# Optimization experiments

Hardware: AMD Instinct MI355X
Metric: run time of the kernel (lower is better)

The kernel has to match this reference:

```python
import jax, jax.numpy as jnp
import numpy as np

B, D = 8192, 256
NUM_CLASSES = 128
CHUNK = 256          # matches module chunk_size; B % CHUNK == 0
TEMP = 0.07
EPS_NORM = 1e-12


def setup_inputs() -> dict:
    key = jax.random.key(0)
    k1, k2 = jax.random.split(key)
    features = jax.random.normal(k1, (B, D), dtype=jnp.float32)
    labels = jax.random.randint(k2, (B,), 0, NUM_CLASSES, dtype=jnp.int64)
    return {"features": features, "labels": labels}


def reference(features, labels):
    n = features.shape[0]
    temperature = max(TEMP, 1e-4)

    # F.normalize(dim=1): x / max(||x||, eps)
    norm = jnp.maximum(jnp.linalg.norm(features, axis=1, keepdims=True), EPS_NORM)
    f = features / norm
    # clamp is a no-op after normalization but kept for faithfulness
    f = jnp.clip(f, -1000.0, 1000.0)

    # [B, B] similarity; the torch loop computes exactly these rows chunk by chunk
    sim = jnp.matmul(f, f.T) / temperature

    # self-mask: each row i masks column i (diagonal of its chunk's square block)
    self_mask = ~jnp.eye(n, dtype=bool)

    # positive mask: same label, excluding self
    pos = (labels[:, None] == labels[None, :]) & self_mask
    # per-chunk fallback: if a 256-row chunk has no positives at all, use self_mask
    pos_c = pos.reshape(n // CHUNK, CHUNK, n)
    has_pos = pos_c.any(axis=(1, 2), keepdims=True)
    pos = jnp.where(has_pos, pos_c, self_mask.reshape(n // CHUNK, CHUNK, n)).reshape(n, n)

    # max-subtract BEFORE self-masking (faithful: includes self-sim = 1/temp)
    sim_max = jnp.max(sim, axis=1, keepdims=True)
    logits = jnp.clip(sim - jax.lax.stop_gradient(sim_max), -1000.0, 1000.0)

    exp_sim = jnp.maximum(jnp.exp(logits), 1e-8) * self_mask
    log_sum_exp = jnp.log(jnp.sum(exp_sim, axis=1, keepdims=True) + 1e-8)
    log_prob = jnp.maximum(logits - log_sum_exp, -1000.0)

    pos_pairs = jnp.sum(pos, axis=1)                      # [B] int
    row_loss = -jnp.sum(pos * log_prob, axis=1)           # [B]
    valid = pos_pairs > 0
    row_loss = jnp.where(valid, row_loss / jnp.maximum(pos_pairs, 1).astype(row_loss.dtype), 0.0)

    total_loss = jnp.sum(row_loss)
    total_pairs = jnp.sum(valid).astype(jnp.float32)
    mean_loss = total_loss / (total_pairs + 1e-8)
    loss = mean_loss  # reduction == 'mean'
    return loss, total_pairs, mean_loss
```

## Files before the change

kernel.cpp:

```cpp
#include <hip/hip_runtime.h>
#include <hip/hip_bf16.h>

#define NB 8192
#define DD 256
#define INV_T (1.0f/0.07f)
#define LOG2E 1.4426950408889634f
#define K1    (INV_T*LOG2E)
#define CEXP  6.2087204553847255e-7f
#define NSTRIP 32
#define TILE 256
#define BN 64
#define BUFB (BN*DD*2)

typedef __attribute__((ext_vector_type(8))) short s8v;
typedef __attribute__((ext_vector_type(4))) float f4v;
typedef unsigned int u32;
typedef unsigned short u16;

#define OFF_FB   0
#define OFF_SEA  (4*1024*1024)
#define OFF_SPA  (OFF_SEA + NB*4)
#define OFF_CE   (OFF_SPA + NB*4)
#define OFF_CP   (OFF_CE + NSTRIP*NB*4)
#define OFF_CL   (OFF_CP + NSTRIP*NB*4)
#define OFF_CV   (OFF_CL + 256)
#define OFF_CNT  (OFF_CV + 256)

__global__ void k_norm(const float* __restrict__ feat,
                       __hip_bfloat16* __restrict__ fb,
                       float* __restrict__ SEa, int* __restrict__ cnt) {
    const int t = threadIdx.x;
    if (blockIdx.x == 0 && t == 0) *cnt = 0;
    if (blockIdx.x < 64) SEa[blockIdx.x * 256 + t] = 0.f;
    const int w = t >> 6, l = t & 63;
    const int row = blockIdx.x * 4 + w;
    const float4 v = ((const float4*)feat)[row * 64 + l];
    float s = v.x * v.x + v.y * v.y + v.z * v.z + v.w * v.w;
    #pragma unroll
    for (int d = 32; d; d >>= 1) s += __shfl_xor(s, d, 64);
    const float scale = 1.0f / fmaxf(sqrtf(s), 1e-12f);
    __hip_bfloat16 h0 = __float2bfloat16(v.x * scale);
    __hip_bfloat16 h1 = __float2bfloat16(v.y * scale);
    __hip_bfloat16 h2 = __float2bfloat16(v.z * scale);
    __hip_bfloat16 h3 = __float2bfloat16(v.w * scale);
    ushort4 o;
    o.x = *(u16*)&h0; o.y = *(u16*)&h1; o.z = *(u16*)&h2; o.w = *(u16*)&h3;
    ((ushort4*)fb)[row * 64 + l] = o;
}

__device__ __forceinline__ void gld16(const void* g, void* l) {
    __builtin_amdgcn_global_load_lds((const __attribute__((address_space(1))) u32*)g,
                                     (__attribute__((address_space(3))) u32*)l, 16, 0, 0);
}

__launch_bounds__(512)
__global__ void k_main(const __hip_bfloat16* __restrict__ fb,
                       const int* __restrict__ lab,
                       float* __restrict__ SEa, float* __restrict__ SPa,
                       float* __restrict__ CE, float* __restrict__ CP) {
    __shared__ __align__(16) char ldsB[2 * BUFB];
    __shared__ float ldsColE[8][BN];
    __shared__ float ldsColP[8][BN];
    const int tid = threadIdx.x;
    const int w = tid >> 6;
    const int l = tid & 63;
    const int l15 = l & 15, lg = l >> 4;

    const int s = blockIdx.x >> 4;
    const int j = blockIdx.x & 15;
    const int nA = 4 * (32 - s);
    const int cnt = 8 + (j >= 12 ? 1 : 0);
    const int off = 8 * j + (j > 12 ? j - 12 : 0);

    s8v a[2][8];
    int labr[8];
    int wbase = 0;
    auto loadA = [&](int r) {
        wbase = r * TILE + w * 32;
        #pragma unroll
        for (int m = 0; m < 2; m++)
            #pragma unroll
            for (int kk = 0; kk < 8; kk++)
                a[m][kk] = *(const s8v*)(fb + (wbase + m * 16 + l15) * DD + kk * 32 + lg * 8);
        #pragma unroll
        for (int m = 0; m < 2; m++)
            #pragma unroll
            for (int r2 = 0; r2 < 4; r2++)
                labr[m * 4 + r2] = lab[wbase + m * 16 + lg * 4 + r2];
    };

    float sE[8], sPa_[8];
    #pragma unroll
    for (int i = 0; i < 8; i++) { sE[i] = 0.f; sPa_[i] = 0.f; }
    auto flushRows = [&]() {
        #pragma unroll
        for (int idx = 0; idx < 8; idx++) {
            #pragma unroll
            for (int d = 1; d < 16; d <<= 1) {
                sE[idx]   += __shfl_xor(sE[idx], d, 16);
                sPa_[idx] += __shfl_xor(sPa_[idx], d, 16);
            }
        }
        if (l15 == 0) {
            #pragma unroll
            for (int idx = 0; idx < 8; idx++) {
                const int row = wbase + (idx >> 2) * 16 + lg * 4 + (idx & 3);
                atomicAdd(&SEa[row], sE[idx]);
                atomicAdd(&SPa[row], sPa_[idx]);
            }
        }
        #pragma unroll
        for (int i = 0; i < 8; i++) { sE[i] = 0.f; sPa_[i] = 0.f; }
    };

    auto stage = [&](int g, int bufoff) {
        const int c0 = (g < nA ? g : g - nA) * 64;
        const char* gt = (const char*)fb + (size_t)c0 * (DD * 2);
        #pragma unroll
        for (int i = 0; i < 4; i++) {
            const int x = i * 8192 + (tid << 4);
            const int br = x >> 9;
            const int inrow = x & 511;
            gld16(gt + br * 512 + (inrow ^ ((br & 7) << 4)),
                  ldsB + bufoff + i * 8192 + w * 1024);
        }
    };

    stage(off, 0);
    loadA(off < nA ? 31 - s : s);
    __syncthreads();

    for (int t = 0; t < cnt; t++) {
        const int g = off + t;
        const int curoff = (t & 1) * BUFB;
        if (t + 1 < cnt) stage(g + 1, curoff ^ BUFB);

        const int r = (g < nA) ? 31 - s : s;
        const int i = (g < nA) ? g : g - nA;
        const int col0 = i * 64;
        const bool diag = ((i >> 2) == r);

        int lc[4];
        #pragma unroll
        for (int n = 0; n < 4; n++)
            lc[n] = lab[col0 + n * 16 + l15];

        f4v acc[2][4];
        #pragma unroll
        for (int m = 0; m < 2; m++)
            #pragma unroll
            for (int n = 0; n < 4; n++)
                acc[m][n] = (f4v){0.f, 0.f, 0.f, 0.f};

        #pragma unroll
        for (int kk = 0; kk < 8; kk++) {
            s8v bfr[4];
            #pragma unroll
            for (int n = 0; n < 4; n++) {
                const int br = n * 16 + l15;
                const int ad = (br * 512 + kk * 64 + lg * 16) ^ ((br & 7) << 4);
                bfr[n] = *(const s8v*)(ldsB + curoff + ad);
            }
            #pragma unroll
            for (int m = 0; m < 2; m++)
                #pragma unroll
                for (int n = 0; n < 4; n++)
                    acc[m][n] = __builtin_amdgcn_mfma_f32_16x16x32_bf16(a[m][kk], bfr[n], acc[m][n], 0, 0, 0);
        }

        float cE[4], cP[4];
        #pragma unroll
        for (int n = 0; n < 4; n++) { cE[n] = 0.f; cP[n] = 0.f; }
        #pragma unroll
        for (int n = 0; n < 4; n++) {
            #pragma unroll
            for (int m = 0; m < 2; m++)
                #pragma unroll
                for (int rr = 0; rr < 4; rr++) {
                    const int idx = m * 4 + rr;
                    const float v = acc[m][n][rr];
                    float e = exp2f(v * K1);
                    bool pos = (lc[n] == labr[idx]);
                    if (diag) {
                        const int row = wbase + m * 16 + lg * 4 + rr;
                        const int coln = col0 + n * 16 + l15;
                        const bool nself = (row != coln);
                        e = nself ? e : 0.f;
                        pos = pos && nself;
                    }
                    const float pv = pos ? v : 0.f;
                    sE[idx] += e;
                    sPa_[idx] += pv;
                    cE[n] += e;
                    cP[n] += pv;
                }
        }

        if (!diag) {
            #pragma unroll
            for (int n = 0; n < 4; n++) {
                cE[n] += __shfl_xor(cE[n], 16, 64);
                cE[n] += __shfl_xor(cE[n], 32, 64);
                cP[n] += __shfl_xor(cP[n], 16, 64);
                cP[n] += __shfl_xor(cP[n], 32, 64);
            }
            if (l < 16) {
                #pragma unroll
                for (int n = 0; n < 4; n++) {
                    ldsColE[w][n * 16 + l15] = cE[n];
                    ldsColP[w][n * 16 + l15] = cP[n];
                }
            }
        }
        __syncthreads();
        if (!diag && tid < BN) {
            float e = 0.f, p = 0.f;
            #pragma unroll
            for (int w2 = 0; w2 < 8; w2++) { e += ldsColE[w2][tid]; p += ldsColP[w2][tid]; }
            CE[r * NB + col0 + tid] = e;
            CP[r * NB + col0 + tid] = p;
        }
        __syncthreads();

        if (t + 1 < cnt && g + 1 == nA) {
            flushRows();
            loadA(s);
        }
    }
    flushRows();
}

__global__ void k_rows(const int* __restrict__ lab,
                       const float* __restrict__ SEa, const float* __restrict__ SPa,
                       const float* __restrict__ CE, const float* __restrict__ CP,
                       float* __restrict__ CL, float* __restrict__ CV,
                       int* __restrict__ cnt, float* __restrict__ out) {
    __shared__ int h[128];
    const int t = threadIdx.x;
    if (t < 128) h[t] = 0;
    __syncthreads();
    #pragma unroll
    for (int i = 0; i < 32; i++)
        atomicAdd(&h[lab[t + i * 256]], 1);
    __syncthreads();

    const int row = blockIdx.x * 256 + t;
    float se = SEa[row], spa = SPa[row];
    for (int r = blockIdx.x + 1; r < NSTRIP; r++) {
        se  += CE[r * NB + row];
        spa += CP[r * NB + row];
    }
    const int n = h[lab[row]] - 1;
    const float lse = logf(se * CEXP + 1e-8f);
    const bool valid = n > 0;
    float loss = valid ? (lse - (spa - (float)n) * INV_T / (float)n) : 0.f;
    float vf = valid ? 1.f : 0.f;
    #pragma unroll
    for (int d = 32; d; d >>= 1) { loss += __shfl_xor(loss, d, 64); vf += __shfl_xor(vf, d, 64); }
    __shared__ float pl[4], pv[4];
    __shared__ int isLast;
    if ((t & 63) == 0) { pl[t >> 6] = loss; pv[t >> 6] = vf; }
    __syncthreads();
    if (t == 0) {
        CL[blockIdx.x] = pl[0] + pl[1] + pl[2] + pl[3];
        CV[blockIdx.x] = pv[0] + pv[1] + pv[2] + pv[3];
        __threadfence();
        isLast = (atomicAdd(cnt, 1) == 31);
    }
    __syncthreads();
    if (isLast) {
        __threadfence();
        float lsum = (t < 32) ? CL[t] : 0.f;
        float vsum = (t < 32) ? CV[t] : 0.f;
        #pragma unroll
        for (int d = 32; d; d >>= 1) { lsum += __shfl_xor(lsum, d, 64); vsum += __shfl_xor(vsum, d, 64); }
        if (t == 0) {
            const float mean = lsum / (vsum + 1e-8f);
            out[0] = mean;
            out[1] = vsum;
            out[2] = mean;
        }
    }
}

extern "C" void kernel_launch(void* const* d_in, const int* in_sizes, int n_in,
                              void* d_out, int out_size, void* d_ws, size_t ws_size,
                              hipStream_t stream) {
    (void)in_sizes; (void)n_in; (void)out_size; (void)ws_size;
    const float* feat = (const float*)d_in[0];
    const int*   lab  = (const int*)d_in[1];
    char* ws = (char*)d_ws;
    __hip_bfloat16* fb = (__hip_bfloat16*)(ws + OFF_FB);
    float* SEa = (float*)(ws + OFF_SEA);
    float* SPa = (float*)(ws + OFF_SPA);
    float* CE  = (float*)(ws + OFF_CE);
    float* CP  = (float*)(ws + OFF_CP);
    float* CL  = (float*)(ws + OFF_CL);
    float* CV  = (float*)(ws + OFF_CV);
    int*   cnt = (int*)(ws + OFF_CNT);
    float* out = (float*)d_out;

    hipLaunchKernelGGL(k_norm, dim3(NB / 4), dim3(256), 0, stream, feat, fb, SEa, cnt);
    hipLaunchKernelGGL(k_main, dim3(256), dim3(512), 0, stream, fb, lab, SEa, SPa, CE, CP);
    hipLaunchKernelGGL(k_rows, dim3(NB / 256), dim3(256), 0, stream, lab, SEa, SPa, CE, CP, CL, CV, cnt, out);
}
```

Before: 71.64 us.

## Compute positive-pair sums via per-class centroid dot products instead of masked tile sums

Replaces the per-element positive-mask accumulation in the main GEMM epilogue with an algebraic identity: the sum of positive similarities for a row equals the dot product of its feature with its class sum, minus its self-dot. Each k_main block now also builds a slice of the per-class feature sums in LDS and adds it into a global buffer with atomics, and k_rows takes the row·centroid dot. This drops the label loads, compares, the extra column-partial buffer CP, and one of the two per-tile barriers, which it replaces with a double-buffered LDS column array. The trade-off is extra atomic traffic and a tail phase in k_main, plus a change in rounding versus the masked sum.

```diff
diff --git a/kernel.cpp b/kernel.cpp
--- a/kernel.cpp
+++ b/kernel.cpp
@@ -19,19 +19,25 @@
 
 #define OFF_FB   0
 #define OFF_SEA  (4*1024*1024)
-#define OFF_SPA  (OFF_SEA + NB*4)
-#define OFF_CE   (OFF_SPA + NB*4)
-#define OFF_CP   (OFF_CE + NSTRIP*NB*4)
-#define OFF_CL   (OFF_CP + NSTRIP*NB*4)
+#define OFF_CE   (OFF_SEA + NB*4)
+#define OFF_C    (OFF_CE + NSTRIP*NB*4)
+#define OFF_CL   (OFF_C + 128*DD*4)
 #define OFF_CV   (OFF_CL + 256)
 #define OFF_CNT  (OFF_CV + 256)
 
+__device__ __forceinline__ float bf2f(short h) {
+    u32 x = ((u32)(u16)h) << 16;
+    return *(float*)&x;
+}
+
 __global__ void k_norm(const float* __restrict__ feat,
                        __hip_bfloat16* __restrict__ fb,
-                       float* __restrict__ SEa, int* __restrict__ cnt) {
+                       float* __restrict__ SEa, float* __restrict__ C,
+                       int* __restrict__ cnt) {
     const int t = threadIdx.x;
     if (blockIdx.x == 0 && t == 0) *cnt = 0;
-    if (blockIdx.x < 64) SEa[blockIdx.x * 256 + t] = 0.f;
+    if (blockIdx.x < 32) SEa[blockIdx.x * 256 + t] = 0.f;
+    else if (blockIdx.x >= 64 && blockIdx.x < 192) C[(blockIdx.x - 64) * 256 + t] = 0.f;
     const int w = t >> 6, l = t & 63;
     const int row = blockIdx.x * 4 + w;
     const float4 v = ((const float4*)feat)[row * 64 + l];
@@ -56,11 +62,10 @@
 __launch_bounds__(512)
 __global__ void k_main(const __hip_bfloat16* __restrict__ fb,
                        const int* __restrict__ lab,
-                       float* __restrict__ SEa, float* __restrict__ SPa,
-                       float* __restrict__ CE, float* __restrict__ CP) {
+                       float* __restrict__ SEa, float* __restrict__ CE,
+                       float* __restrict__ C) {
     __shared__ __align__(16) char ldsB[2 * BUFB];
-    __shared__ float ldsColE[8][BN];
-    __shared__ float ldsColP[8][BN];
+    __shared__ float ldsCol[2][8][BN];
     const int tid = threadIdx.x;
     const int w = tid >> 6;
     const int l = tid & 63;
@@ -73,7 +78,6 @@
     const int off = 8 * j + (j > 12 ? j - 12 : 0);
 
     s8v a[2][8];
-    int labr[8];
     int wbase = 0;
     auto loadA = [&](int r) {
         wbase = r * TILE + w * 32;
@@ -82,35 +86,26 @@
             #pragma unroll
             for (int kk = 0; kk < 8; kk++)
                 a[m][kk] = *(const s8v*)(fb + (wbase + m * 16 + l15) * DD + kk * 32 + lg * 8);
-        #pragma unroll
-        for (int m = 0; m < 2; m++)
-            #pragma unroll
-            for (int r2 = 0; r2 < 4; r2++)
-                labr[m * 4 + r2] = lab[wbase + m * 16 + lg * 4 + r2];
     };
 
-    float sE[8], sPa_[8];
-    #pragma unroll
-    for (int i = 0; i < 8; i++) { sE[i] = 0.f; sPa_[i] = 0.f; }
+    float sE[8];
+    #pragma unroll
+    for (int i = 0; i < 8; i++) sE[i] = 0.f;
     auto flushRows = [&]() {
         #pragma unroll
-        for (int idx = 0; idx < 8; idx++) {
-            #pragma unroll
-            for (int d = 1; d < 16; d <<= 1) {
-                sE[idx]   += __shfl_xor(sE[idx], d, 16);
-                sPa_[idx] += __shfl_xor(sPa_[idx], d, 16);
-            }
-        }
+        for (int idx = 0; idx < 8; idx++)
+            #pragma unroll
+            for (int d = 1; d < 16; d <<= 1)
+                sE[idx] += __shfl_xor(sE[idx], d, 16);
         if (l15 == 0) {
             #pragma unroll
             for (int idx = 0; idx < 8; idx++) {
                 const int row = wbase + (idx >> 2) * 16 + lg * 4 + (idx & 3);
                 atomicAdd(&SEa[row], sE[idx]);
-                atomicAdd(&SPa[row], sPa_[idx]);
             }
         }
         #pragma unroll
-        for (int i = 0; i < 8; i++) { sE[i] = 0.f; sPa_[i] = 0.f; }
+        for (int i = 0; i < 8; i++) sE[i] = 0.f;
     };
 
     auto stage = [&](int g, int bufoff) {
@@ -140,11 +135,6 @@
         const int col0 = i * 64;
         const bool diag = ((i >> 2) == r);
 
-        int lc[4];
-        #pragma unroll
-        for (int n = 0; n < 4; n++)
-            lc[n] = lab[col0 + n * 16 + l15];
-
         f4v acc[2][4];
         #pragma unroll
         for (int m = 0; m < 2; m++)
@@ -168,32 +158,25 @@
                     acc[m][n] = __builtin_amdgcn_mfma_f32_16x16x32_bf16(a[m][kk], bfr[n], acc[m][n], 0, 0, 0);
         }
 
-        float cE[4], cP[4];
-        #pragma unroll
-        for (int n = 0; n < 4; n++) { cE[n] = 0.f; cP[n] = 0.f; }
+        float cE[4];
         #pragma unroll
         for (int n = 0; n < 4; n++) {
+            float cEn = 0.f;
             #pragma unroll
             for (int m = 0; m < 2; m++)
                 #pragma unroll
                 for (int rr = 0; rr < 4; rr++) {
                     const int idx = m * 4 + rr;
-                    const float v = acc[m][n][rr];
-                    float e = exp2f(v * K1);
-                    bool pos = (lc[n] == labr[idx]);
+                    float e = exp2f(acc[m][n][rr] * K1);
                     if (diag) {
                         const int row = wbase + m * 16 + lg * 4 + rr;
                         const int coln = col0 + n * 16 + l15;
-                        const bool nself = (row != coln);
-                        e = nself ? e : 0.f;
-                        pos = pos && nself;
+                        e = (row != coln) ? e : 0.f;
                     }
-                    const float pv = pos ? v : 0.f;
                     sE[idx] += e;
-                    sPa_[idx] += pv;
-                    cE[n] += e;
-                    cP[n] += pv;
+                    cEn += e;
                 }
+            cE[n] = cEn;
         }
 
         if (!diag) {
@@ -201,26 +184,20 @@
             for (int n = 0; n < 4; n++) {
                 cE[n] += __shfl_xor(cE[n], 16, 64);
                 cE[n] += __shfl_xor(cE[n], 32, 64);
-                cP[n] += __shfl_xor(cP[n], 16, 64);
-                cP[n] += __shfl_xor(cP[n], 32, 64);
             }
             if (l < 16) {
                 #pragma unroll
-                for (int n = 0; n < 4; n++) {
-                    ldsColE[w][n * 16 + l15] = cE[n];
-                    ldsColP[w][n * 16 + l15] = cP[n];
-                }
+                for (int n = 0; n < 4; n++)
+                    ldsCol[t & 1][w][n * 16 + l15] = cE[n];
             }
         }
         __syncthreads();
         if (!diag && tid < BN) {
-            float e = 0.f, p = 0.f;
-            #pragma unroll
-            for (int w2 = 0; w2 < 8; w2++) { e += ldsColE[w2][tid]; p += ldsColP[w2][tid]; }
+            float e = 0.f;
+            #pragma unroll
+            for (int w2 = 0; w2 < 8; w2++) e += ldsCol[t & 1][w2][tid];
             CE[r * NB + col0 + tid] = e;
-            CP[r * NB + col0 + tid] = p;
-        }
-        __syncthreads();
+        }
 
         if (t + 1 < cnt && g + 1 == nA) {
             flushRows();
@@ -228,11 +205,40 @@
         }
     }
     flushRows();
-}
-
-__global__ void k_rows(const int* __restrict__ lab,
-                       const float* __restrict__ SEa, const float* __restrict__ SPa,
-                       const float* __restrict__ CE, const float* __restrict__ CP,
+
+    __syncthreads();
+    float* accW = (float*)ldsB;
+    for (int i = tid; i < 8192; i += 512) accW[i] = 0.f;
+    __syncthreads();
+    {
+        const int rbase = (blockIdx.x >> 5) * 1024 + w * 128;
+        const int d0 = (blockIdx.x & 31) * 8;
+        #pragma unroll
+        for (int k = 0; k < 2; k++) {
+            const int row = rbase + k * 64 + l;
+            const s8v v = *(const s8v*)(fb + row * DD + d0);
+            const int c = lab[row];
+            #pragma unroll
+            for (int d = 0; d < 8; d++)
+                atomicAdd(&accW[(w * 128 + c) * 8 + d], bf2f(v[d]));
+        }
+    }
+    __syncthreads();
+    {
+        const int d0 = (blockIdx.x & 31) * 8;
+        for (int i = tid; i < 1024; i += 512) {
+            const int c = i >> 3, d = i & 7;
+            float sum = 0.f;
+            #pragma unroll
+            for (int w2 = 0; w2 < 8; w2++) sum += accW[(w2 * 128 + c) * 8 + d];
+            atomicAdd(&C[c * DD + d0 + d], sum);
+        }
+    }
+}
+
+__global__ void k_rows(const int* __restrict__ lab, const __hip_bfloat16* __restrict__ fb,
+                       const float* __restrict__ SEa, const float* __restrict__ CE,
+                       const float* __restrict__ C,
                        float* __restrict__ CL, float* __restrict__ CV,
                        int* __restrict__ cnt, float* __restrict__ out) {
     __shared__ int h[128];
@@ -245,11 +251,26 @@
     __syncthreads();
 
     const int row = blockIdx.x * 256 + t;
-    float se = SEa[row], spa = SPa[row];
-    for (int r = blockIdx.x + 1; r < NSTRIP; r++) {
-        se  += CE[r * NB + row];
-        spa += CP[r * NB + row];
-    }
+    float se = SEa[row];
+    for (int r = blockIdx.x + 1; r < NSTRIP; r++)
+        se += CE[r * NB + row];
+
+    const s8v* fi8 = (const s8v*)(fb + row * DD);
+    const float4* Cl4 = (const float4*)(C + lab[row] * DD);
+    float spa = 0.f, selfdot = 0.f;
+    #pragma unroll
+    for (int q = 0; q < 32; q++) {
+        const s8v v = fi8[q];
+        const float4 ca = Cl4[2 * q], cb = Cl4[2 * q + 1];
+        const float f0 = bf2f(v[0]), f1 = bf2f(v[1]), f2 = bf2f(v[2]), f3 = bf2f(v[3]);
+        const float f4 = bf2f(v[4]), f5 = bf2f(v[5]), f6 = bf2f(v[6]), f7 = bf2f(v[7]);
+        spa += f0 * ca.x + f1 * ca.y + f2 * ca.z + f3 * ca.w
+             + f4 * cb.x + f5 * cb.y + f6 * cb.z + f7 * cb.w;
+        selfdot += f0 * f0 + f1 * f1 + f2 * f2 + f3 * f3
+                 + f4 * f4 + f5 * f5 + f6 * f6 + f7 * f7;
+    }
+    spa -= selfdot;
+
     const int n = h[lab[row]] - 1;
     const float lse = logf(se * CEXP + 1e-8f);
     const bool valid = n > 0;
@@ -292,15 +313,14 @@
     char* ws = (char*)d_ws;
     __hip_bfloat16* fb = (__hip_bfloat16*)(ws + OFF_FB);
     float* SEa = (float*)(ws + OFF_SEA);
-    float* SPa = (float*)(ws + OFF_SPA);
     float* CE  = (float*)(ws + OFF_CE);
-    float* CP  = (float*)(ws + OFF_CP);
+    float* C   = (float*)(ws + OFF_C);
     float* CL  = (float*)(ws + OFF_CL);
     float* CV  = (float*)(ws + OFF_CV);
     int*   cnt = (int*)(ws + OFF_CNT);
     float* out = (float*)d_out;
 
-    hipLaunchKernelGGL(k_norm, dim3(NB / 4), dim3(256), 0, stream, feat, fb, SEa, cnt);
-    hipLaunchKernelGGL(k_main, dim3(256), dim3(512), 0, stream, fb, lab, SEa, SPa, CE, CP);
-    hipLaunchKernelGGL(k_rows, dim3(NB / 256), dim3(256), 0, stream, lab, SEa, SPa, CE, CP, CL, CV, cnt, out);
-}
+    hipLaunchKernelGGL(k_norm, dim3(NB / 4), dim3(256), 0, stream, feat, fb, SEa, C, cnt);
+    hipLaunchKernelGGL(k_main, dim3(256), dim3(512), 0, stream, fb, lab, SEa, CE, C);
+    hipLaunchKernelGGL(k_rows, dim3(NB / 256), dim3(256), 0, stream, lab, fb, SEa, CE, C, CL, CV, cnt, out);
+}
```

After: 104.8 us. 1.46x slower.
